# Optimization experiments

Hardware: AMD Instinct MI355X
Metric: run time of the kernel (lower is better)

The kernel has to match this reference:

```python
import jax, jax.numpy as jnp
import numpy as np

B, S, D, K = 16384, 50, 512, 5  # batch, pred_horizon(=steps), dec_units, components_n
H = S  # time_stamp width equals pred_horizon


def setup_inputs() -> dict:
    key = jax.random.key(0)
    ks = jax.random.split(key, 13)
    sc = 0.05
    f32 = jnp.float32
    return {
        "conditions": jax.random.normal(ks[0], (B, S, 3), f32),
        "state_h": jax.random.normal(ks[1], (B, D), f32),
        "state_c": jax.random.normal(ks[2], (B, D), f32),
        # merger LSTM (input = enc_h[D] ++ cond[3])
        "W_m": jax.random.normal(ks[3], (D + 3, 4 * D), f32) * sc,
        "U_m": jax.random.normal(ks[4], (D, 4 * D), f32) * sc,
        "b_m": jnp.zeros((4 * D,), f32),
        # merger MDN heads packed: [alphas|mus_long|sigmas_long|mus_lat|sigmas_lat|rhos]
        "Wh_m": jax.random.normal(ks[5], (D + H, 6 * K), f32) * sc,
        "bh_m": jnp.zeros((6 * K,), f32),
        # yielder LSTM
        "W_y": jax.random.normal(ks[6], (D + 3, 4 * D), f32) * sc,
        "U_y": jax.random.normal(ks[7], (D, 4 * D), f32) * sc,
        "b_y": jnp.zeros((4 * D,), f32),
        # yielder MDN heads packed: [alphas|mus_long|sigmas_long]
        "Wh_y": jax.random.normal(ks[8], (D + H, 3 * K), f32) * sc,
        "bh_y": jnp.zeros((3 * K,), f32),
    }


def _lstm_step(x, h, c, W, U, b):
    # Keras LSTM gate order: i, f, g(cell), o
    z = x @ W + h @ U + b
    i, f, g, o = jnp.split(z, 4, axis=-1)
    c2 = jax.nn.sigmoid(f) * c + jax.nn.sigmoid(i) * jnp.tanh(g)
    h2 = jax.nn.sigmoid(o) * jnp.tanh(c2)
    return h2, c2


def reference(conditions, state_h, state_c, W_m, U_m, b_m, Wh_m, bh_m,
              W_y, U_y, b_y, Wh_y, bh_y):
    # time_stamp[s] = ones in [:s+1] (lower-triangular)
    time_stamp = jnp.tril(jnp.ones((S, H), conditions.dtype))
    enc_h = state_h  # re-fed every step, [B, D]
    # With teacher_percent=1.0 both merger and yielder step conditions are
    # conditions[:, t, :3] at step t (step 0 also uses t=0).
    conds_t = jnp.transpose(conditions, (1, 0, 2))  # [S, B, 3]

    def step(carry, xs):
        h_m, c_m, h_y, c_y = carry
        cond_t, ts = xs  # [B,3], [H]
        x_in = jnp.concatenate([enc_h, cond_t], axis=-1)  # [B, D+3]
        ts_b = jnp.broadcast_to(ts, (h_m.shape[0], H))
        # merger vehicle
        h_m, c_m = _lstm_step(x_in, h_m, c_m, W_m, U_m, b_m)
        feat_m = jnp.concatenate([h_m, ts_b], axis=-1)  # [B, D+H]
        zm = feat_m @ Wh_m + bh_m
        a, ml, sl, mlt, slt, r = jnp.split(zm, 6, axis=-1)
        pm = jnp.concatenate([jax.nn.softmax(a, axis=-1), ml, jnp.exp(sl),
                              mlt, jnp.exp(slt), jnp.tanh(r)], axis=-1)  # [B,30]
        # yielder vehicle
        h_y, c_y = _lstm_step(x_in, h_y, c_y, W_y, U_y, b_y)
        feat_y = jnp.concatenate([h_y, ts_b], axis=-1)
        zy = feat_y @ Wh_y + bh_y
        ay, mly, sly = jnp.split(zy, 3, axis=-1)
        py = jnp.concatenate([jax.nn.softmax(ay, axis=-1), mly, jnp.exp(sly)], axis=-1)  # [B,15]
        return (h_m, c_m, h_y, c_y), (pm, py)

    carry0 = (state_h, state_c, state_h, state_c)
    _, (param_m, param_y) = jax.lax.scan(step, carry0, (conds_t, time_stamp))
    param_m = jnp.transpose(param_m, (1, 0, 2))  # [B, S, 30]
    param_y = jnp.transpose(param_y, (1, 0, 2))  # [B, S, 15]
    return param_m, param_y
```

## Files before the change

### kernel.cpp

```cpp
#include <hip/hip_runtime.h>

typedef __bf16 bf16;
typedef __attribute__((ext_vector_type(8))) __bf16 bf16x8;
typedef __attribute__((ext_vector_type(4))) __bf16 bf16x4;
typedef __attribute__((ext_vector_type(4))) float f32x4;
typedef __attribute__((ext_vector_type(4))) int i32x4;

#define B_TOT 16384
#define SEQ 50
#define DH 512
#define ZW 2048
#define NT 16
#define NGEMM 4096
#define NITEM 4352

#define MFMA16(a, b, c) __builtin_amdgcn_mfma_f32_16x16x32_bf16(a, b, c, 0, 0, 0)

__device__ __forceinline__ float fsigm(float x) {
    return __fdividef(1.0f, 1.0f + __expf(-x));
}
__device__ __forceinline__ float ftanh(float x) {
    float e = __expf(2.0f * x);
    return 1.0f - __fdividef(2.0f, e + 1.0f);
}


__global__ void init_state(const float* __restrict__ sh,
                           bf16* __restrict__ h0m, bf16* __restrict__ h0y) {
    size_t i = (size_t)blockIdx.x * 256 + threadIdx.x;
    int row = i >> 9, k = i & 511;
    size_t off = (((size_t)(row >> 4) * 16 + (k >> 5)) * 64 + ((k >> 3) & 3) * 16 +
                  (row & 15)) * 8 + (k & 7);
    bf16 hb = (bf16)sh[i];
    h0m[off] = hb;
    h0y[off] = hb;
}

__global__ void build_c3(const float* __restrict__ src,
                         float* __restrict__ dM, float* __restrict__ dY) {
    size_t i = (size_t)blockIdx.x * 256 + threadIdx.x;
    int row = i >> 9, hcol = i & 511;
    float v = src[i];
    size_t o = ((size_t)(row >> 2) * 512 + hcol) * 4 + (row & 3);
    dM[o] = v;
    dY[o] = v;
}

__device__ __forceinline__ int orig_col(int colp) {
    return ((colp >> 4) & 3) * 512 + ((colp >> 6) << 4) + (colp & 15);
}

__global__ void reorder_weights(const float* __restrict__ Um, const float* __restrict__ Uy,
                                const float* __restrict__ Wm, const float* __restrict__ Wy,
                                bf16* __restrict__ UtM, bf16* __restrict__ UtY,
                                bf16* __restrict__ WtM, bf16* __restrict__ WtY) {
    int idx = blockIdx.x * 256 + threadIdx.x;
    int which = idx >> 20;
    int r = idx & ((1 << 20) - 1);
    int colp = r >> 9, k = r & 511;
    int orig = orig_col(colp);
    const float* src = which == 0 ? Um : which == 1 ? Uy : which == 2 ? Wm : Wy;
    bf16* dst = which == 0 ? UtM : which == 1 ? UtY : which == 2 ? WtM : WtY;
    int cb = colp >> 4, fr = colp & 15;
    int kt = k >> 5, fq = (k >> 3) & 3, e = k & 7;
    int lane = fq * 16 + fr;
    dst[(((size_t)(cb * 16 + kt) * 64 + lane) << 3) + e] = (bf16)src[(size_t)k * ZW + orig];
}

__global__ void build_wc2(const float* __restrict__ Wm, const float* __restrict__ Wy,
                          float* __restrict__ Wc2M, float* __restrict__ Wc2Y) {
    int idx = blockIdx.x * 256 + threadIdx.x;
    if (idx >= 2 * 512 * 12) return;
    int which = idx / 6144;
    int r2 = idx % 6144;
    int hcol = r2 / 12, rg = r2 % 12;
    int r = rg >> 2, g = rg & 3;
    const float* src = which ? Wy : Wm;
    float* dst = which ? Wc2Y : Wc2M;
    dst[hcol * 12 + rg] = src[(size_t)(512 + r) * ZW + g * 512 + hcol];
}

__global__ void cond_transpose(const float* __restrict__ cond, float* __restrict__ condT4) {
    int idx = blockIdx.x * 256 + threadIdx.x;
    if (idx >= SEQ * B_TOT) return;
    int t = idx / B_TOT, row = idx % B_TOT;
    const float* s = cond + ((size_t)row * SEQ + t) * 3;
    f32x4 v = {s[0], s[1], s[2], 0.f};
    *(f32x4*)(condT4 + (size_t)idx * 4) = v;
}

__global__ void build_heads(const float* __restrict__ Whm, const float* __restrict__ bhm,
                            const float* __restrict__ Why, const float* __restrict__ bhy,
                            bf16* __restrict__ WhmT, bf16* __restrict__ WhyT,
                            float* __restrict__ tscm, float* __restrict__ tscy) {
    int i = blockIdx.x * 256 + threadIdx.x;
    const int N1 = 32 * 512, N2 = 16 * 512, N3 = SEQ * 32, N4 = SEQ * 16;
    if (i < N1) {
        int n = i >> 9, k = i & 511;
        WhmT[i] = (bf16)(n < 30 ? Whm[k * 30 + n] : 0.f);
    } else if (i < N1 + N2) {
        int j = i - N1;
        int n = j >> 9, k = j & 511;
        WhyT[j] = (bf16)(n < 15 ? Why[k * 15 + n] : 0.f);
    } else if (i < N1 + N2 + N3) {
        int j = i - (N1 + N2);
        int tt = j >> 5, col = j & 31;
        float v = 0.f;
        if (col < 30) {
            v = bhm[col];
            for (int s = 0; s <= tt; ++s) v += Whm[(512 + s) * 30 + col];
        }
        tscm[j] = v;
    } else if (i < N1 + N2 + N3 + N4) {
        int j = i - (N1 + N2 + N3);
        int tt = j >> 4, col = j & 15;
        float v = 0.f;
        if (col < 15) {
            v = bhy[col];
            for (int s = 0; s <= tt; ++s) v += Why[(512 + s) * 15 + col];
        }
        tscy[j] = v;
    }
}


struct DecP {
    bf16 *hM0, *hM1, *hY0, *hY1;
    const bf16 *UtM, *UtY, *WtM, *WtY;
    bf16 *xwM, *xwY;
    const float *Wc2M, *Wc2Y, *bm, *by_;
    float *cM, *cY;
    const float* condT4;
    const bf16 *WhmT, *WhyT;
    const float *tscm, *tscy;
    float* out;
};

#define WAIT_VM(n)                                                  \
    do {                                                            \
        asm volatile("s_waitcnt vmcnt(" #n ")" ::: "memory");       \
        __builtin_amdgcn_sched_barrier(0);                          \
    } while (0)

template <int MODE>
__device__ __forceinline__ void gemm_item(const DecP& P, int item, int t) {
    const int tid = threadIdx.x;
    const int wave = tid >> 6, lane = tid & 63;
    const int bz = item >> 11;
    const int lin = item & 2047;
    const int xcd = lin & 7, jj2 = lin >> 3;
    const int bx = xcd * 16 + (jj2 >> 4);
    const int by = jj2 & 15;
    const int brow = bx * 128;

    const bf16* A;
    const bf16* Bt;
    if (MODE == 0) {
        A = P.hM0;
        Bt = bz ? P.WtY : P.WtM;
    } else {
        A = bz ? ((t & 1) ? P.hY1 : P.hY0) : ((t & 1) ? P.hM1 : P.hM0);
        Bt = bz ? P.UtY : P.UtM;
    }

    const int fr = lane & 15, fq = lane >> 4;
    const int wr = wave >> 1, wc = wave & 1;

    const uint64_t abase =
        (uint64_t)(const char*)A + (uint64_t)(bx * 8 + wr * 4) * 16384 + lane * 16;
    const uint64_t bbase =
        (uint64_t)(const char*)Bt + (uint64_t)(by * 8 + wc * 4) * 16384 + lane * 16;

    f32x4 acc[4][4];
#pragma unroll
    for (int m = 0; m < 4; ++m)
#pragma unroll
        for (int n = 0; n < 4; ++n) acc[m][n] = (f32x4){0.f, 0.f, 0.f, 0.f};

    i32x4 afr[4][4], bfr[4][4];

#define AGLOAD(bank, kts)                                                         \
    do {                                                                          \
        uint64_t _a = abase + (uint64_t)(kts) * 1024;                             \
        asm volatile("global_load_dwordx4 %0, %1, off"                            \
                     : "=&v"(afr[bank][0]) : "v"(_a) : "memory");                 \
        asm volatile("global_load_dwordx4 %0, %1, off"                            \
                     : "=&v"(afr[bank][1]) : "v"(_a + 16384) : "memory");         \
        asm volatile("global_load_dwordx4 %0, %1, off"                            \
                     : "=&v"(afr[bank][2]) : "v"(_a + 32768) : "memory");         \
        asm volatile("global_load_dwordx4 %0, %1, off"                            \
                     : "=&v"(afr[bank][3]) : "v"(_a + 49152) : "memory");         \
    } while (0)
#define BGLOAD(bank, kts)                                                         \
    do {                                                                          \
        uint64_t _b = bbase + (uint64_t)(kts) * 1024;                             \
        asm volatile("global_load_dwordx4 %0, %1, off"                            \
                     : "=&v"(bfr[bank][0]) : "v"(_b) : "memory");                 \
        asm volatile("global_load_dwordx4 %0, %1, off"                            \
                     : "=&v"(bfr[bank][1]) : "v"(_b + 16384) : "memory");         \
        asm volatile("global_load_dwordx4 %0, %1, off"                            \
                     : "=&v"(bfr[bank][2]) : "v"(_b + 32768) : "memory");         \
        asm volatile("global_load_dwordx4 %0, %1, off"                            \
                     : "=&v"(bfr[bank][3]) : "v"(_b + 49152) : "memory");         \
    } while (0)

    AGLOAD(0, 0);
    BGLOAD(0, 0);
    AGLOAD(1, 1);
    BGLOAD(1, 1);
    AGLOAD(2, 2);
    BGLOAD(2, 2);
    AGLOAD(3, 3);
    BGLOAD(3, 3);

#pragma unroll
    for (int kt = 0; kt < NT; ++kt) {
        if (kt < NT - 3) {
            WAIT_VM(24);
        } else if (kt == NT - 3) {
            WAIT_VM(16);
        } else if (kt == NT - 2) {
            WAIT_VM(8);
        } else {
            WAIT_VM(0);
        }
        __builtin_amdgcn_s_setprio(1);
#pragma unroll
        for (int m = 0; m < 4; ++m)
#pragma unroll
            for (int n = 0; n < 4; ++n)
                acc[m][n] = MFMA16(__builtin_bit_cast(bf16x8, afr[kt & 3][m]),
                                   __builtin_bit_cast(bf16x8, bfr[kt & 3][n]), acc[m][n]);
        __builtin_amdgcn_s_setprio(0);
        __builtin_amdgcn_sched_barrier(0);
        if (kt + 4 < NT) {
            AGLOAD(kt & 3, kt + 4);
            BGLOAD(kt & 3, kt + 4);
        }
    }
#undef AGLOAD
#undef BGLOAD

    const int jb = by * 2 + wc;
    const int hcol = jb * 16 + fr;
    const int rowbase = brow + wr * 64 + fq * 4;
    const int rb0 = (rowbase >> 2);

    if (MODE == 0) {
        const float* bias = bz ? P.by_ : P.bm;
        bf16* XO = bz ? P.xwY : P.xwM;
        float b0 = bias[hcol], b1 = bias[512 + hcol], b2 = bias[1024 + hcol],
              b3 = bias[1536 + hcol];
#pragma unroll
        for (int m = 0; m < 4; ++m) {
            bf16x8 v0, v1;
#pragma unroll
            for (int j = 0; j < 2; ++j) {
                v0[j * 4 + 0] = (bf16)(acc[m][0][j] + b0);
                v0[j * 4 + 1] = (bf16)(acc[m][1][j] + b1);
                v0[j * 4 + 2] = (bf16)(acc[m][2][j] + b2);
                v0[j * 4 + 3] = (bf16)(acc[m][3][j] + b3);
            }
#pragma unroll
            for (int j = 2; j < 4; ++j) {
                v1[(j - 2) * 4 + 0] = (bf16)(acc[m][0][j] + b0);
                v1[(j - 2) * 4 + 1] = (bf16)(acc[m][1][j] + b1);
                v1[(j - 2) * 4 + 2] = (bf16)(acc[m][2][j] + b2);
                v1[(j - 2) * 4 + 3] = (bf16)(acc[m][3][j] + b3);
            }
            bf16* o = XO + ((size_t)(rb0 + m * 4) * 512 + hcol) * 16;
            *(bf16x8*)(o) = v0;
            *(bf16x8*)(o + 8) = v1;
        }
    } else {
        float* Cb = bz ? P.cY : P.cM;
        bf16* Ho = bz ? (((t + 1) & 1) ? P.hY1 : P.hY0)
                      : (((t + 1) & 1) ? P.hM1 : P.hM0);
        const bf16* xw = bz ? P.xwY : P.xwM;
        const float* Wc2 = bz ? P.Wc2Y : P.Wc2M;
        f32x4 wcv0 = *(const f32x4*)(Wc2 + hcol * 12);
        f32x4 wcv1 = *(const f32x4*)(Wc2 + hcol * 12 + 4);
        f32x4 wcv2 = *(const f32x4*)(Wc2 + hcol * 12 + 8);
        const int ktc = jb >> 1;
        const int fqp = (jb & 1) * 2 + (fr >> 3);
        bf16* hob = Ho + (((size_t)((brow >> 4) + wr * 4) * 16 + ktc) * 64 + fqp * 16 +
                          fq * 4) * 8 + (fr & 7);
#pragma unroll
        for (int m = 0; m < 4; ++m) {
            const size_t co = ((size_t)(rb0 + m * 4) * 512 + hcol);
            const bf16* xp = xw + co * 16;
            bf16x8 xv0 = *(const bf16x8*)(xp);
            bf16x8 xv1 = *(const bf16x8*)(xp + 8);
            f32x4 cvm = *(const f32x4*)(Cb + co * 4);
            const int row0 = rowbase + m * 16;
            f32x4 cd[4];
#pragma unroll
            for (int j = 0; j < 4; ++j)
                cd[j] = *(const f32x4*)(P.condT4 + ((size_t)t * B_TOT + row0 + j) * 4);
            f32x4 cnew;
            bf16* hom = hob + (size_t)m * 16 * 64 * 8;
#pragma unroll
            for (int j = 0; j < 4; ++j) {
                float z[4];
#pragma unroll
                for (int g = 0; g < 4; ++g) {
                    float xwv = (j < 2) ? (float)xv0[j * 4 + g] : (float)xv1[(j - 2) * 4 + g];
                    z[g] = acc[m][g][j] + xwv + cd[j][0] * wcv0[g] + cd[j][1] * wcv1[g] +
                           cd[j][2] * wcv2[g];
                }
                float ii = fsigm(z[0]);
                float ff = fsigm(z[1]);
                float gg = ftanh(z[2]);
                float oo = fsigm(z[3]);
                float cn = ff * cvm[j] + ii * gg;
                cnew[j] = cn;
                hom[j * 8] = (bf16)(oo * ftanh(cn));
            }
            *(f32x4*)(Cb + co * 4) = cnew;
        }
    }
}

__device__ __forceinline__ void heads_item(const DecP& P, float* zbuf, int hb, int th) {
    const int tid = threadIdx.x, wave = tid >> 6, lane = tid & 63;
    const int fr = lane & 15, fq = lane >> 4;
    const int rbase = hb * 64 + wave * 16;
    const int rg = rbase >> 4;
    const int a = (th + 1) & 1;
    const bf16* hm = a ? P.hM1 : P.hM0;
    const bf16* hy = a ? P.hY1 : P.hY0;

    f32x4 am0 = {0.f, 0.f, 0.f, 0.f}, am1 = {0.f, 0.f, 0.f, 0.f}, ay0 = {0.f, 0.f, 0.f, 0.f};

    for (int kt = 0; kt < 16; ++kt) {
        const size_t ao = ((size_t)(rg * 16 + kt) * 64 + lane) * 8;
        bf16x8 a0 = *(const bf16x8*)(hm + ao);
        bf16x8 y0 = *(const bf16x8*)(hy + ao);
        const int k0 = kt * 32;
        const size_t bo = (size_t)fr * DH + k0 + fq * 8;
        bf16x8 b0 = *(const bf16x8*)(P.WhmT + bo);
        bf16x8 b1 = *(const bf16x8*)(P.WhmT + bo + 16 * DH);
        bf16x8 yb = *(const bf16x8*)(P.WhyT + bo);
        am0 = MFMA16(a0, b0, am0);
        am1 = MFMA16(a0, b1, am1);
        ay0 = MFMA16(y0, yb, ay0);
    }

    float* zm = zbuf + wave * 768;
    float* zy = zm + 512;
#pragma unroll
    for (int j = 0; j < 4; ++j) {
        int rl = fq * 4 + j;
        zm[rl * 32 + fr] = am0[j] + P.tscm[th * 32 + fr];
        zm[rl * 32 + 16 + fr] = am1[j] + P.tscm[th * 32 + 16 + fr];
        zy[rl * 16 + fr] = ay0[j] + P.tscy[th * 16 + fr];
    }
    __syncthreads();

    const int r = lane & 15;
    const size_t grow = (size_t)rbase + r;
    if (lane < 16) {
        float z[30];
#pragma unroll
        for (int i = 0; i < 30; ++i) z[i] = zm[r * 32 + i];
        float* o = P.out + (grow * SEQ + th) * 30;
        float mx = z[0];
#pragma unroll
        for (int i = 1; i < 5; ++i) mx = fmaxf(mx, z[i]);
        float e[5], s = 0.f;
#pragma unroll
        for (int i = 0; i < 5; ++i) {
            e[i] = __expf(z[i] - mx);
            s += e[i];
        }
        float inv = __fdividef(1.f, s);
#pragma unroll
        for (int i = 0; i < 5; ++i) o[i] = e[i] * inv;
#pragma unroll
        for (int i = 5; i < 10; ++i) o[i] = z[i];
#pragma unroll
        for (int i = 10; i < 15; ++i) o[i] = __expf(z[i]);
#pragma unroll
        for (int i = 15; i < 20; ++i) o[i] = z[i];
#pragma unroll
        for (int i = 20; i < 25; ++i) o[i] = __expf(z[i]);
#pragma unroll
        for (int i = 25; i < 30; ++i) o[i] = ftanh(z[i]);
    } else if (lane < 32) {
        float z[15];
#pragma unroll
        for (int i = 0; i < 15; ++i) z[i] = zy[r * 16 + i];
        float* o = P.out + (size_t)B_TOT * SEQ * 30 + (grow * SEQ + th) * 15;
        float mx = z[0];
#pragma unroll
        for (int i = 1; i < 5; ++i) mx = fmaxf(mx, z[i]);
        float e[5], s = 0.f;
#pragma unroll
        for (int i = 0; i < 5; ++i) {
            e[i] = __expf(z[i] - mx);
            s += e[i];
        }
        float inv = __fdividef(1.f, s);
#pragma unroll
        for (int i = 0; i < 5; ++i) o[i] = e[i] * inv;
#pragma unroll
        for (int i = 5; i < 10; ++i) o[i] = z[i];
#pragma unroll
        for (int i = 10; i < 15; ++i) o[i] = __expf(z[i]);
    }
}

__global__ __launch_bounds__(256, 2) void step_kernel(DecP P, int t, int itemOff) {
    __shared__ float zbuf[4 * 768];
    const int item = blockIdx.x + itemOff;
    if (item < NGEMM) {
        if (t < 0)
            gemm_item<0>(P, item, 0);
        else if (t < SEQ)
            gemm_item<1>(P, item, t);
    } else if (item < NITEM) {
        if (t >= 1) heads_item(P, zbuf, item - NGEMM, t - 1);
    }
}

extern "C" void kernel_launch(void* const* d_in, const int* in_sizes, int n_in,
                              void* d_out, int out_size, void* d_ws, size_t ws_size,
                              hipStream_t stream) {
    const float* cond = (const float*)d_in[0];
    const float* sh = (const float*)d_in[1];
    const float* sc = (const float*)d_in[2];
    const float* Wm = (const float*)d_in[3];
    const float* Um = (const float*)d_in[4];
    const float* bm = (const float*)d_in[5];
    const float* Whm = (const float*)d_in[6];
    const float* bhm = (const float*)d_in[7];
    const float* Wy = (const float*)d_in[8];
    const float* Uy = (const float*)d_in[9];
    const float* by_ = (const float*)d_in[10];
    const float* Why = (const float*)d_in[11];
    const float* bhy = (const float*)d_in[12];
    float* out = (float*)d_out;

    char* p = (char*)d_ws;
    auto take = [&](size_t bytes) {
        char* r = p;
        p += (bytes + 255) & ~(size_t)255;
        return r;
    };
    bf16* UtM = (bf16*)take((size_t)ZW * DH * 2);
    bf16* UtY = (bf16*)take((size_t)ZW * DH * 2);
    bf16* WtM = (bf16*)take((size_t)ZW * DH * 2);
    bf16* WtY = (bf16*)take((size_t)ZW * DH * 2);
    float* Wc2M = (float*)take(512 * 12 * 4);
    float* Wc2Y = (float*)take(512 * 12 * 4);
    bf16* WhmT = (bf16*)take(32 * DH * 2);
    bf16* WhyT = (bf16*)take(16 * DH * 2);
    float* tscm = (float*)take(SEQ * 32 * 4);
    float* tscy = (float*)take(SEQ * 16 * 4);
    float* condT4 = (float*)take((size_t)SEQ * B_TOT * 4 * 4);
    bf16* xwM = (bf16*)take((size_t)B_TOT * ZW * 2);
    bf16* xwY = (bf16*)take((size_t)B_TOT * ZW * 2);
    bf16* hM0 = (bf16*)take((size_t)B_TOT * DH * 2);
    bf16* hM1 = (bf16*)take((size_t)B_TOT * DH * 2);
    bf16* hY0 = (bf16*)take((size_t)B_TOT * DH * 2);
    bf16* hY1 = (bf16*)take((size_t)B_TOT * DH * 2);
    float* cMb = (float*)take((size_t)B_TOT * DH * 4);
    float* cYb = (float*)take((size_t)B_TOT * DH * 4);

    init_state<<<(B_TOT * DH) / 256, 256, 0, stream>>>(sh, hM0, hY0);
    build_c3<<<(B_TOT * DH) / 256, 256, 0, stream>>>(sc, cMb, cYb);
    reorder_weights<<<(4 * ZW * DH) / 256, 256, 0, stream>>>(Um, Uy, Wm, Wy, UtM, UtY, WtM, WtY);
    build_wc2<<<(2 * 512 * 12 + 255) / 256, 256, 0, stream>>>(Wm, Wy, Wc2M, Wc2Y);
    cond_transpose<<<(SEQ * B_TOT + 255) / 256, 256, 0, stream>>>(cond, condT4);
    build_heads<<<(32 * 512 + 16 * 512 + SEQ * 32 + SEQ * 16 + 255) / 256, 256, 0, stream>>>(
        Whm, bhm, Why, bhy, WhmT, WhyT, tscm, tscy);

    DecP P;
    P.hM0 = hM0;
    P.hM1 = hM1;
    P.hY0 = hY0;
    P.hY1 = hY1;
    P.UtM = UtM;
    P.UtY = UtY;
    P.WtM = WtM;
    P.WtY = WtY;
    P.xwM = xwM;
    P.xwY = xwY;
    P.Wc2M = Wc2M;
    P.Wc2Y = Wc2Y;
    P.bm = bm;
    P.by_ = by_;
    P.cM = cMb;
    P.cY = cYb;
    P.condT4 = condT4;
    P.WhmT = WhmT;
    P.WhyT = WhyT;
    P.tscm = tscm;
    P.tscy = tscy;
    P.out = out;

    step_kernel<<<NGEMM, 256, 0, stream>>>(P, -1, 0);
    for (int t = 0; t < SEQ; ++t)
        step_kernel<<<NITEM, 256, 0, stream>>>(P, t, 0);
    step_kernel<<<NITEM - NGEMM, 256, 0, stream>>>(P, SEQ, NGEMM);
}
```

Baseline: 6.975 ms.

## Split batch into two row chunks and run full recurrence per chunk

The batch is split into two halves of 8192 rows, and the full 50-step recurrence is run for each half in turn, with each step launching half as many GEMM and head blocks. The aim is to keep the per-chunk hidden/cell state and activations resident in the L2/MALL cache across steps, reducing DRAM traffic. In exchange it doubles the number of kernel launches and halves the parallelism of each launch, which may leave compute units underused.

```diff
diff --git a/kernel.cpp b/kernel.cpp
--- a/kernel.cpp
+++ b/kernel.cpp
@@ -11,8 +11,12 @@
 #define DH 512
 #define ZW 2048
 #define NT 16
-#define NGEMM 4096
-#define NITEM 4352
+
+#define NCHUNK 2
+#define CROWS 8192
+#define NG0 4096
+#define NG1 2048
+#define NH1 128
 
 #define MFMA16(a, b, c) __builtin_amdgcn_mfma_f32_16x16x32_bf16(a, b, c, 0, 0, 0)
 
@@ -143,15 +147,15 @@
     } while (0)
 
 template <int MODE>
-__device__ __forceinline__ void gemm_item(const DecP& P, int item, int t) {
+__device__ __forceinline__ void gemm_item(const DecP& P, int item, int t, int rowOff) {
     const int tid = threadIdx.x;
     const int wave = tid >> 6, lane = tid & 63;
-    const int bz = item >> 11;
-    const int lin = item & 2047;
+    const int bz = (MODE == 0) ? (item >> 11) : (item >> 10);
+    const int lin = (MODE == 0) ? (item & 2047) : (item & 1023);
     const int xcd = lin & 7, jj2 = lin >> 3;
-    const int bx = xcd * 16 + (jj2 >> 4);
+    const int bx = (MODE == 0) ? (xcd * 16 + (jj2 >> 4)) : (xcd * 8 + (jj2 >> 4));
     const int by = jj2 & 15;
-    const int brow = bx * 128;
+    const int brow = rowOff + bx * 128;
 
     const bf16* A;
     const bf16* Bt;
@@ -167,7 +171,7 @@
     const int wr = wave >> 1, wc = wave & 1;
 
     const uint64_t abase =
-        (uint64_t)(const char*)A + (uint64_t)(bx * 8 + wr * 4) * 16384 + lane * 16;
+        (uint64_t)(const char*)A + (uint64_t)((brow >> 4) + wr * 4) * 16384 + lane * 16;
     const uint64_t bbase =
         (uint64_t)(const char*)Bt + (uint64_t)(by * 8 + wc * 4) * 16384 + lane * 16;
 
@@ -321,10 +325,11 @@
     }
 }
 
-__device__ __forceinline__ void heads_item(const DecP& P, float* zbuf, int hb, int th) {
+__device__ __forceinline__ void heads_item(const DecP& P, float* zbuf, int hb, int th,
+                                           int rowOff) {
     const int tid = threadIdx.x, wave = tid >> 6, lane = tid & 63;
     const int fr = lane & 15, fq = lane >> 4;
-    const int rbase = hb * 64 + wave * 16;
+    const int rbase = rowOff + hb * 64 + wave * 16;
     const int rg = rbase >> 4;
     const int a = (th + 1) & 1;
     const bf16* hm = a ? P.hM1 : P.hM0;
@@ -410,16 +415,17 @@
     }
 }
 
-__global__ __launch_bounds__(256, 2) void step_kernel(DecP P, int t, int itemOff) {
+__global__ __launch_bounds__(256, 2) void step_kernel(DecP P, int t, int itemOff,
+                                                      int rowOff, int ngemm) {
     __shared__ float zbuf[4 * 768];
     const int item = blockIdx.x + itemOff;
-    if (item < NGEMM) {
+    if (item < ngemm) {
         if (t < 0)
-            gemm_item<0>(P, item, 0);
+            gemm_item<0>(P, item, 0, 0);
         else if (t < SEQ)
-            gemm_item<1>(P, item, t);
-    } else if (item < NITEM) {
-        if (t >= 1) heads_item(P, zbuf, item - NGEMM, t - 1);
+            gemm_item<1>(P, item, t, rowOff);
+    } else {
+        if (t >= 1) heads_item(P, zbuf, item - ngemm, t - 1, rowOff);
     }
 }
 
@@ -499,8 +505,12 @@
     P.tscy = tscy;
     P.out = out;
 
-    step_kernel<<<NGEMM, 256, 0, stream>>>(P, -1, 0);
-    for (int t = 0; t < SEQ; ++t)
-        step_kernel<<<NITEM, 256, 0, stream>>>(P, t, 0);
-    step_kernel<<<NITEM - NGEMM, 256, 0, stream>>>(P, SEQ, NGEMM);
-}
+    step_kernel<<<NG0, 256, 0, stream>>>(P, -1, 0, 0, NG0);
+
+    for (int ch = 0; ch < NCHUNK; ++ch) {
+        const int rowOff = ch * CROWS;
+        for (int t = 0; t < SEQ; ++t)
+            step_kernel<<<NG1 + NH1, 256, 0, stream>>>(P, t, 0, rowOff, NG1);
+        step_kernel<<<NH1, 256, 0, stream>>>(P, SEQ, NG1, rowOff, NG1);
+    }
+}
```

Result: faster. 6.801 ms (-2.5%).
